# Kernel tuning notes

Hardware: AMD Instinct MI355X
Metric: run time of the kernel (lower is better)

Reference implementation:

```python
import jax, jax.numpy as jnp
import numpy as np

V, D, H, L, B, S = 8192, 128, 8, 2, 1, 128
HD = D // H
HID = int(8 * D / 3)
EPS = 1e-6


def setup_inputs() -> dict:
    key = jax.random.key(0)
    ks = jax.random.split(key, 12)
    sc = 0.02
    return {
        "idx": jax.random.randint(ks[0], (B, S), 0, V),
        "w_raw": jax.random.normal(ks[1], (D, V), jnp.float32) * sc,
        "norm1_w": jnp.ones((L, D), jnp.float32),
        "norm2_w": jnp.ones((L, D), jnp.float32),
        "wq": jax.random.normal(ks[2], (L, D, D), jnp.float32) * sc,
        "wk": jax.random.normal(ks[3], (L, D, D), jnp.float32) * sc,
        "wv": jax.random.normal(ks[4], (L, D, D), jnp.float32) * sc,
        "wo": jax.random.normal(ks[5], (L, D, D), jnp.float32) * sc,
        "w1": jax.random.normal(ks[6], (L, D, HID), jnp.float32) * sc,
        "w3": jax.random.normal(ks[7], (L, D, HID), jnp.float32) * sc,
        "w2": jax.random.normal(ks[8], (L, HID, D), jnp.float32) * sc,
        "final_norm_w": jnp.ones((D,), jnp.float32),
    }


def rmsnorm(x, w):
    return x * jax.lax.rsqrt(jnp.mean(x * x, axis=-1, keepdims=True) + EPS) * w


def rope_cos_sin(seqlen, hd):
    inv = 1.0 / (10000.0 ** (jnp.arange(0, hd, 2, dtype=jnp.float32) / hd))
    t = jnp.arange(seqlen, dtype=jnp.float32)
    f = jnp.outer(t, inv)  # (S, hd/2)
    return jnp.cos(f), jnp.sin(f)


def apply_rope(x, cos, sin):
    # x: (B,S,H,HD); interleaved complex pairs as in Llama
    x0, x1 = x[..., 0::2], x[..., 1::2]
    c = cos[None, :, None, :]
    s = sin[None, :, None, :]
    r0 = x0 * c - x1 * s
    r1 = x0 * s + x1 * c
    return jnp.stack([r0, r1], axis=-1).reshape(x.shape)


def forward(idx, w_raw, norm1_w, norm2_w, wq, wk, wv, wo, w1, w2, w3, final_norm_w):
    Wemb = jax.nn.sigmoid(w_raw)                 # (D,V)
    x = Wemb.T[idx]                              # Yoneda one-hot @ W.T == gather -> (B,S,D)
    cos, sin = rope_cos_sin(S, HD)
    causal = jnp.tril(jnp.ones((S, S), bool))[None, None]  # (1,1,S,S)
    scale = 1.0 / jnp.sqrt(jnp.float32(HD))
    for i in range(L):
        # Multi-Universe attention (heads == universes), RoPE, causal SDPA
        h = rmsnorm(x, norm1_w[i])
        q = (h @ wq[i]).reshape(B, S, H, HD)
        k = (h @ wk[i]).reshape(B, S, H, HD)
        v = (h @ wv[i]).reshape(B, S, H, HD)
        q = apply_rope(q, cos, sin)
        k = apply_rope(k, cos, sin)
        scores = jnp.einsum("bihd,bjhd->bhij", q, k) * scale
        scores = jnp.where(causal, scores, jnp.float32(-1e9))
        attn = jax.nn.softmax(scores, axis=-1)
        o = jnp.einsum("bhij,bjhd->bihd", attn, v).reshape(B, S, D) @ wo[i]
        x = x + o
        # SwiGLU FFN
        h2 = rmsnorm(x, norm2_w[i])
        x = x + (jax.nn.silu(h2 @ w1[i]) * (h2 @ w3[i])) @ w2[i]
    x_norm = rmsnorm(x, final_norm_w)
    # Godel-Heyting reachability head
    x_n = x_norm / jnp.linalg.norm(x_norm, axis=-1, keepdims=True)      # (B,S,D)
    v_n = (Wemb / jnp.linalg.norm(Wemb, axis=0, keepdims=True)).T        # (V,D)
    a = x_n[:, :, None, :]                                               # (B,S,1,D)
    b = v_n[None, None, :, :]                                            # (1,1,V,D)
    # strict Godel implication: a => b = 1 if a <= b else b
    imp = jnp.where(a <= b, jnp.float32(1.0), b)                         # (B,S,V,D)
    logits = jnp.clip(imp.mean(axis=-1), 1e-6, 1.0 - 1e-6)               # (B,S,V)
    return logits


def reference(idx, w_raw, norm1_w, norm2_w, wq, wk, wv, wo, w1, w2, w3, final_norm_w):
    return forward(idx, w_raw, norm1_w, norm2_w, wq, wk, wv, wo, w1, w2, w3, final_norm_w)
```

## Files before the change

kernel.cpp:

```cpp
#include <hip/hip_runtime.h>
#include <math.h>

#define V 8192
#define D 128
#define NH 8
#define HD 16
#define SEQ 128
#define HID 341
#define EPS 1e-6f

__device__ __forceinline__ float sigm(float x) { return 1.0f / (1.0f + expf(-x)); }

__device__ __forceinline__ float block_sum256(float v, float* scratch) {
    #pragma unroll
    for (int m = 32; m > 0; m >>= 1) v += __shfl_xor(v, m);
    if ((threadIdx.x & 63) == 0) scratch[threadIdx.x >> 6] = v;
    __syncthreads();
    float s = (scratch[0] + scratch[1]) + (scratch[2] + scratch[3]);
    __syncthreads();
    return s;
}

__device__ __forceinline__ void qkv_rope(const float* hr, const float* wq,
                                         const float* wk, const float* wv, int s,
                                         float* qrow, float* krow,
                                         float (*vpart)[D], float* qo, float* ko,
                                         float* vo) {
    int t = threadIdx.x;
    int col = t & 127, half = t >> 7;
    {
        const float* w = (t < 128) ? wq : wk;
        float a0 = 0, a1 = 0;
        #pragma unroll 8
        for (int d = 0; d < D; d += 2) {
            a0 += hr[d] * w[d * D + col];
            a1 += hr[d + 1] * w[(d + 1) * D + col];
        }
        if (t < 128) qrow[col] = a0 + a1;
        else krow[col] = a0 + a1;
    }
    {
        int dlo = half * 64;
        float a0 = 0, a1 = 0;
        #pragma unroll 8
        for (int d = dlo; d < dlo + 64; d += 2) {
            a0 += hr[d] * wv[d * D + col];
            a1 += hr[d + 1] * wv[(d + 1) * D + col];
        }
        vpart[half][col] = a0 + a1;
    }
    __syncthreads();
    if (t < 128) {
        vo[s * D + t] = vpart[0][t] + vpart[1][t];
        int c = t & (HD - 1);
        int m = c >> 1;
        float fr = (float)s * expf(-(float)m * 1.15129254649702283e+00f);
        float cs = cosf(fr), sn = sinf(fr);
        int base = t & ~1;
        float qe = qrow[base], qod = qrow[base + 1];
        float ke = krow[base], kod = krow[base + 1];
        qo[s * D + t] = (c & 1) ? (qe * sn + qod * cs) : (qe * cs - qod * sn);
        ko[s * D + t] = (c & 1) ? (ke * sn + kod * cs) : (ke * cs - kod * sn);
    }
}

__global__ __launch_bounds__(256) void k_embed_qkv(
    const int* __restrict__ idx, const float* __restrict__ w_raw,
    const float* __restrict__ wq, const float* __restrict__ wk,
    const float* __restrict__ wv, const float* __restrict__ n1w,
    float* __restrict__ x, float* __restrict__ q, float* __restrict__ k,
    float* __restrict__ v) {
    __shared__ float hr[D], qrow[D], krow[D], vpart[2][D], scr[4];
    int s = blockIdx.x, t = threadIdx.x;
    float xv = 0.f;
    if (t < 128) {
        xv = sigm(w_raw[t * V + idx[s]]);
        x[s * D + t] = xv;
    }
    float ss = block_sum256(xv * xv, scr);
    float r = 1.0f / sqrtf(ss * (1.0f / D) + EPS);
    if (t < 128) hr[t] = xv * r * n1w[t];
    __syncthreads();
    qkv_rope(hr, wq, wk, wv, s, qrow, krow, vpart, q, k, v);
}

template <int MODE>
__global__ __launch_bounds__(256) void k_layer(
    const float* __restrict__ q, const float* __restrict__ kg,
    const float* __restrict__ vg, float* __restrict__ x,
    const float* __restrict__ wo, const float* __restrict__ n2w,
    const float* __restrict__ w1, const float* __restrict__ w3,
    const float* __restrict__ w2, const float* __restrict__ wq,
    const float* __restrict__ wk, const float* __restrict__ wv,
    const float* __restrict__ n1w, float* __restrict__ qo, float* __restrict__ ko,
    float* __restrict__ vo, const float* __restrict__ fw, float* __restrict__ xng) {
    __shared__ float ps[NH][SEQ + 1];
    __shared__ float qs[D], orow[D], h2[D];
    __shared__ float part[2][D];
    __shared__ float qrow[D], krow[D];
    __shared__ float afA[HID], afB[HID], af[HID];
    __shared__ float rl[NH];
    __shared__ float scr[4];
    int s = blockIdx.x, t = threadIdx.x;
    int col = t & 127, half = t >> 7;

    float xr = 0.f;
    if (t < 128) {
        qs[t] = q[s * D + t];
        xr = x[s * D + t];
    }
    __syncthreads();

    {
        int j = col;
        #pragma unroll
        for (int u = 0; u < 4; ++u) {
            int h = half + 2 * u;
            const float4* kp = (const float4*)&kg[j * D + h * HD];
            float4 ka = kp[0], kb = kp[1], kc = kp[2], kd = kp[3];
            const float* qh = &qs[h * HD];
            float acc = ka.x * qh[0] + ka.y * qh[1] + ka.z * qh[2] + ka.w * qh[3] +
                        kb.x * qh[4] + kb.y * qh[5] + kb.z * qh[6] + kb.w * qh[7] +
                        kc.x * qh[8] + kc.y * qh[9] + kc.z * qh[10] + kc.w * qh[11] +
                        kd.x * qh[12] + kd.y * qh[13] + kd.z * qh[14] + kd.w * qh[15];
            ps[h][j] = acc * 0.25f;
        }
    }
    __syncthreads();

    {
        int h = t >> 5, lane = t & 31;
        float pm = -1e30f;
        for (int j = lane; j <= s; j += 32) pm = fmaxf(pm, ps[h][j]);
        #pragma unroll
        for (int m = 16; m > 0; m >>= 1) pm = fmaxf(pm, __shfl_xor(pm, m, 32));
        float psum = 0.f;
        for (int j = lane; j <= s; j += 32) {
            float e = expf(ps[h][j] - pm);
            ps[h][j] = e;
            psum += e;
        }
        #pragma unroll
        for (int m = 16; m > 0; m >>= 1) psum += __shfl_xor(psum, m, 32);
        if (lane == 0) rl[h] = 1.0f / psum;
    }
    __syncthreads();

    {
        int h = col >> 4;
        int jlo = half * 64;
        int jhi = (s < jlo + 63) ? s : (jlo + 63);
        float a0 = 0, a1 = 0, a2 = 0, a3 = 0;
        int j = jlo;
        #pragma unroll 4
        for (; j + 3 <= jhi; j += 4) {
            a0 += ps[h][j] * vg[j * D + col];
            a1 += ps[h][j + 1] * vg[(j + 1) * D + col];
            a2 += ps[h][j + 2] * vg[(j + 2) * D + col];
            a3 += ps[h][j + 3] * vg[(j + 3) * D + col];
        }
        for (; j <= jhi; ++j) a0 += ps[h][j] * vg[j * D + col];
        part[half][col] = (a0 + a1) + (a2 + a3);
    }
    __syncthreads();
    if (t < 128) orow[t] = (part[0][t] + part[1][t]) * rl[t >> 4];
    __syncthreads();

    {
        int dlo = half * 64;
        float a0 = 0, a1 = 0;
        #pragma unroll 8
        for (int d = dlo; d < dlo + 64; d += 2) {
            a0 += orow[d] * wo[d * D + col];
            a1 += orow[d + 1] * wo[(d + 1) * D + col];
        }
        part[half][col] = a0 + a1;
    }
    __syncthreads();
    float xn = 0.f;
    if (t < 128) xn = xr + part[0][t] + part[1][t];
    float ss2 = block_sum256((t < 128) ? xn * xn : 0.f, scr);
    float r2 = 1.0f / sqrtf(ss2 * (1.0f / D) + EPS);
    if (t < 128) h2[t] = xn * r2 * n2w[t];
    __syncthreads();

    for (int task = t; task < 2 * HID; task += 256) {
        int mat = task >= HID;
        int c2 = mat ? (task - HID) : task;
        const float* w = mat ? w3 : w1;
        float a0 = 0, a1 = 0;
        #pragma unroll 8
        for (int d = 0; d < D; d += 2) {
            a0 += h2[d] * w[d * HID + c2];
            a1 += h2[d + 1] * w[(d + 1) * HID + c2];
        }
        if (mat) afB[c2] = a0 + a1;
        else afA[c2] = a0 + a1;
    }
    __syncthreads();
    for (int c2 = t; c2 < HID; c2 += 256) {
        float a1v = afA[c2];
        af[c2] = (a1v / (1.0f + expf(-a1v))) * afB[c2];
    }
    __syncthreads();

    {
        int lo = half * 171;
        int hi = half ? HID : 171;
        float a0 = 0, a1 = 0;
        int tt = lo;
        #pragma unroll 8
        for (; tt + 1 < hi; tt += 2) {
            a0 += af[tt] * w2[tt * D + col];
            a1 += af[tt + 1] * w2[(tt + 1) * D + col];
        }
        for (; tt < hi; ++tt) a0 += af[tt] * w2[tt * D + col];
        part[half][col] = a0 + a1;
    }
    __syncthreads();
    float x2 = 0.f;
    if (t < 128) {
        x2 = xn + part[0][t] + part[1][t];
        if (MODE == 0) x[s * D + t] = x2;
    }

    if constexpr (MODE == 0) {
        float ss = block_sum256((t < 128) ? x2 * x2 : 0.f, scr);
        float r = 1.0f / sqrtf(ss * (1.0f / D) + EPS);
        if (t < 128) h2[t] = x2 * r * n1w[t];
        __syncthreads();
        qkv_rope(h2, wq, wk, wv, s, qrow, krow, part, qo, ko, vo);
    } else {
        float ss = block_sum256((t < 128) ? x2 * x2 : 0.f, scr);
        float r = 1.0f / sqrtf(ss * (1.0f / D) + EPS);
        float y = (t < 128) ? x2 * r * fw[t] : 0.f;
        float nn = block_sum256(y * y, scr);
        if (t < 128) xng[t * SEQ + s] = y / sqrtf(nn);
    }
}

__global__ __launch_bounds__(256) void k_logits(const float* __restrict__ xng,
                                                const float* __restrict__ w_raw,
                                                float* __restrict__ out) {
    __shared__ float xs[D * 64];
    __shared__ float vs[D * 32];
    __shared__ float nred[256];
    __shared__ float invn_s[32];
    int t = threadIdx.x;
    int sbase = (blockIdx.x & 1) * 64;
    int vbase = (blockIdx.x >> 1) * 32;
    for (int i = t; i < D * 64; i += 256) {
        int d = i >> 6, s2 = i & 63;
        xs[i] = xng[d * SEQ + sbase + s2];
    }
    for (int i = t; i < D * 32; i += 256) {
        int d = i >> 5, jj = i & 31;
        vs[i] = sigm(w_raw[d * V + vbase + jj]);
    }
    __syncthreads();
    {
        int colc = t & 31, dp = t >> 5;
        float p = 0.f;
        for (int u = 0; u < 16; ++u) {
            float vv = vs[(dp * 16 + u) * 32 + colc];
            p += vv * vv;
        }
        nred[t] = p;
    }
    __syncthreads();
    if (t < 32) {
        float sum = 0.f;
        for (int u = 0; u < 8; ++u) sum += nred[u * 32 + t];
        invn_s[t] = 1.0f / sqrtf(sum);
    }
    __syncthreads();
    for (int i = t; i < D * 32; i += 256) vs[i] *= invn_s[i & 31];
    __syncthreads();
    int vg = t & 15;
    int sg = t >> 4;
    float acc[4][2] = {};
    for (int d = 0; d < D; ++d) {
        float4 xq = *(const float4*)&xs[d * 64 + sg * 4];
        float2 vq = *(const float2*)&vs[d * 32 + vg * 2];
        acc[0][0] += (xq.x <= vq.x) ? 1.0f : vq.x;
        acc[0][1] += (xq.x <= vq.y) ? 1.0f : vq.y;
        acc[1][0] += (xq.y <= vq.x) ? 1.0f : vq.x;
        acc[1][1] += (xq.y <= vq.y) ? 1.0f : vq.y;
        acc[2][0] += (xq.z <= vq.x) ? 1.0f : vq.x;
        acc[2][1] += (xq.z <= vq.y) ? 1.0f : vq.y;
        acc[3][0] += (xq.w <= vq.x) ? 1.0f : vq.x;
        acc[3][1] += (xq.w <= vq.y) ? 1.0f : vq.y;
    }
    const float inv128 = 1.0f / 128.0f;
    #pragma unroll
    for (int si = 0; si < 4; ++si) {
        int s = sbase + sg * 4 + si;
        float2 ov;
        ov.x = fminf(fmaxf(acc[si][0] * inv128, 1e-6f), 1.0f - 1e-6f);
        ov.y = fminf(fmaxf(acc[si][1] * inv128, 1e-6f), 1.0f - 1e-6f);
        *(float2*)&out[s * V + vbase + vg * 2] = ov;
    }
}

extern "C" void kernel_launch(void* const* d_in, const int* in_sizes, int n_in,
                              void* d_out, int out_size, void* d_ws, size_t ws_size,
                              hipStream_t stream) {
    const int* idx = (const int*)d_in[0];
    const float* w_raw = (const float*)d_in[1];
    const float* n1w = (const float*)d_in[2];
    const float* n2w = (const float*)d_in[3];
    const float* wq = (const float*)d_in[4];
    const float* wk = (const float*)d_in[5];
    const float* wv = (const float*)d_in[6];
    const float* wo = (const float*)d_in[7];
    const float* w1 = (const float*)d_in[8];
    const float* w3 = (const float*)d_in[9];
    const float* w2 = (const float*)d_in[10];
    const float* fnw = (const float*)d_in[11];
    float* out = (float*)d_out;
    float* ws = (float*)d_ws;

    float* x   = ws;
    float* q1  = ws + 16384;
    float* k1  = ws + 32768;
    float* v1  = ws + 49152;
    float* q2  = ws + 65536;
    float* k2  = ws + 81920;
    float* v2  = ws + 98304;
    float* xng = ws + 114688;

    k_embed_qkv<<<dim3(SEQ), dim3(256), 0, stream>>>(idx, w_raw, wq, wk, wv, n1w,
                                                     x, q1, k1, v1);
    k_layer<0><<<dim3(SEQ), dim3(256), 0, stream>>>(
        q1, k1, v1, x, wo, n2w, w1, w3, w2,
        wq + D * D, wk + D * D, wv + D * D, n1w + D, q2, k2, v2,
        (const float*)nullptr, (float*)nullptr);
    k_layer<1><<<dim3(SEQ), dim3(256), 0, stream>>>(
        q2, k2, v2, x, wo + D * D, n2w + D, w1 + D * HID, w3 + D * HID,
        w2 + HID * D, (const float*)nullptr, (const float*)nullptr,
        (const float*)nullptr, (const float*)nullptr, (float*)nullptr,
        (float*)nullptr, (float*)nullptr, fnw, xng);
    k_logits<<<dim3(512), dim3(256), 0, stream>>>(xng, w_raw, out);
}
```

Measured before the change: 159.2 us.

## Coalesce matvecs with float4 loads and shared atomics, precompute vocab norms, prefetch weights

```diff
diff --git a/kernel.cpp b/kernel.cpp
--- a/kernel.cpp
+++ b/kernel.cpp
@@ -9,7 +9,8 @@
 #define HID 341
 #define EPS 1e-6f
 
-__device__ __forceinline__ float sigm(float x) { return 1.0f / (1.0f + expf(-x)); }
+__device__ __forceinline__ float sigm(float x) { return 1.0f / (1.0f + __expf(-x)); }
+__device__ __forceinline__ float silu(float x) { return x / (1.0f + __expf(-x)); }
 
 __device__ __forceinline__ float block_sum256(float v, float* scratch) {
     #pragma unroll
@@ -21,71 +22,98 @@
     return s;
 }
 
-__device__ __forceinline__ void qkv_rope(const float* hr, const float* wq,
-                                         const float* wk, const float* wv, int s,
-                                         float* qrow, float* krow,
-                                         float (*vpart)[D], float* qo, float* ko,
-                                         float* vo) {
+__global__ __launch_bounds__(256, 1) void k_embed_qkv(
+    const int* __restrict__ idx, const float* __restrict__ w_raw,
+    const float* __restrict__ wq, const float* __restrict__ wk,
+    const float* __restrict__ wv, const float* __restrict__ n1w,
+    const float* __restrict__ w1, const float* __restrict__ w3,
+    const float* __restrict__ w2, const float* __restrict__ wo,
+    float* __restrict__ x, float* __restrict__ q, float* __restrict__ k,
+    float* __restrict__ v, float* __restrict__ invn, float* __restrict__ sink) {
     int t = threadIdx.x;
-    int col = t & 127, half = t >> 7;
-    {
-        const float* w = (t < 128) ? wq : wk;
-        float a0 = 0, a1 = 0;
-        #pragma unroll 8
-        for (int d = 0; d < D; d += 2) {
-            a0 += hr[d] * w[d * D + col];
-            a1 += hr[d + 1] * w[(d + 1) * D + col];
-        }
-        if (t < 128) qrow[col] = a0 + a1;
-        else krow[col] = a0 + a1;
-    }
-    {
-        int dlo = half * 64;
-        float a0 = 0, a1 = 0;
-        #pragma unroll 8
-        for (int d = dlo; d < dlo + 64; d += 2) {
-            a0 += hr[d] * wv[d * D + col];
-            a1 += hr[d + 1] * wv[(d + 1) * D + col];
-        }
-        vpart[half][col] = a0 + a1;
-    }
-    __syncthreads();
-    if (t < 128) {
-        vo[s * D + t] = vpart[0][t] + vpart[1][t];
+    if (blockIdx.x >= SEQ) {
+        int vbase = (blockIdx.x - SEQ) * 32;
+        int vloc = t >> 3, dp = t & 7;
+        int vv = vbase + vloc;
+        float acc = 0.f;
+        #pragma unroll
+        for (int u = 0; u < 16; ++u) {
+            float val = sigm(w_raw[(dp * 16 + u) * V + vv]);
+            acc += val * val;
+        }
+        #pragma unroll
+        for (int m = 1; m < 8; m <<= 1) acc += __shfl_xor(acc, m);
+        if (dp == 0) invn[vv] = 1.0f / sqrtf(acc);
+        int g = (blockIdx.x - SEQ) * 256 + t;
+        float wa = 0.f;
+        if (g < 21824) {
+            float4 u1 = ((const float4*)w1)[g]; wa += u1.x + u1.y + u1.z + u1.w;
+            float4 u3 = ((const float4*)w3)[g]; wa += u3.x + u3.y + u3.z + u3.w;
+            float4 u2 = ((const float4*)w2)[g]; wa += u2.x + u2.y + u2.z + u2.w;
+        }
+        if (g < 8192) {
+            float4 a = ((const float4*)wq)[g]; wa += a.x + a.y + a.z + a.w;
+            float4 b = ((const float4*)wk)[g]; wa += b.x + b.y + b.z + b.w;
+            float4 c = ((const float4*)wv)[g]; wa += c.x + c.y + c.z + c.w;
+            float4 d = ((const float4*)wo)[g]; wa += d.x + d.y + d.z + d.w;
+        }
+        if (wa == 1234.5678f) sink[0] = wa;
+        return;
+    }
+    __shared__ float h2[D], qacc[D], kacc[D], vacc[D], scr[4];
+    int s = blockIdx.x;
+    if (t < 128) { qacc[t] = 0.f; kacc[t] = 0.f; vacc[t] = 0.f; }
+    float xv = 0.f;
+    if (t < 128) {
+        xv = sigm(w_raw[t * V + idx[s]]);
+        x[s * D + t] = xv;
+    }
+    float ss = block_sum256(xv * xv, scr);
+    float r = 1.0f / sqrtf(ss * (1.0f / D) + EPS);
+    if (t < 128) h2[t] = xv * r * n1w[t];
+    __syncthreads();
+    {
+        const float4* q4 = (const float4*)wq;
+        const float4* k4 = (const float4*)wk;
+        const float4* v4 = (const float4*)wv;
+        float qa0 = 0, qa1 = 0, qa2 = 0, qa3 = 0;
+        float ka0 = 0, ka1 = 0, ka2 = 0, ka3 = 0;
+        float va0 = 0, va1 = 0, va2 = 0, va3 = 0;
+        #pragma unroll 4
+        for (int j = 0; j < 16; ++j) {
+            int i4 = t + 256 * j;
+            int row = i4 >> 5;
+            float hv = h2[row];
+            float4 a = q4[i4], b = k4[i4], c = v4[i4];
+            qa0 += hv * a.x; qa1 += hv * a.y; qa2 += hv * a.z; qa3 += hv * a.w;
+            ka0 += hv * b.x; ka1 += hv * b.y; ka2 += hv * b.z; ka3 += hv * b.w;
+            va0 += hv * c.x; va1 += hv * c.y; va2 += hv * c.z; va3 += hv * c.w;
+        }
+        int c0 = (t & 31) * 4;
+        atomicAdd(&qacc[c0], qa0); atomicAdd(&qacc[c0 + 1], qa1);
+        atomicAdd(&qacc[c0 + 2], qa2); atomicAdd(&qacc[c0 + 3], qa3);
+        atomicAdd(&kacc[c0], ka0); atomicAdd(&kacc[c0 + 1], ka1);
+        atomicAdd(&kacc[c0 + 2], ka2); atomicAdd(&kacc[c0 + 3], ka3);
+        atomicAdd(&vacc[c0], va0); atomicAdd(&vacc[c0 + 1], va1);
+        atomicAdd(&vacc[c0 + 2], va2); atomicAdd(&vacc[c0 + 3], va3);
+    }
+    __syncthreads();
+    if (t < 128) {
+        v[s * D + t] = vacc[t];
         int c = t & (HD - 1);
         int m = c >> 1;
         float fr = (float)s * expf(-(float)m * 1.15129254649702283e+00f);
         float cs = cosf(fr), sn = sinf(fr);
         int base = t & ~1;
-        float qe = qrow[base], qod = qrow[base + 1];
-        float ke = krow[base], kod = krow[base + 1];
-        qo[s * D + t] = (c & 1) ? (qe * sn + qod * cs) : (qe * cs - qod * sn);
-        ko[s * D + t] = (c & 1) ? (ke * sn + kod * cs) : (ke * cs - kod * sn);
+        float qe = qacc[base], qod = qacc[base + 1];
+        float ke = kacc[base], kod = kacc[base + 1];
+        q[s * D + t] = (c & 1) ? (qe * sn + qod * cs) : (qe * cs - qod * sn);
+        k[s * D + t] = (c & 1) ? (ke * sn + kod * cs) : (ke * cs - kod * sn);
     }
 }
 
-__global__ __launch_bounds__(256) void k_embed_qkv(
-    const int* __restrict__ idx, const float* __restrict__ w_raw,
-    const float* __restrict__ wq, const float* __restrict__ wk,
-    const float* __restrict__ wv, const float* __restrict__ n1w,
-    float* __restrict__ x, float* __restrict__ q, float* __restrict__ k,
-    float* __restrict__ v) {
-    __shared__ float hr[D], qrow[D], krow[D], vpart[2][D], scr[4];
-    int s = blockIdx.x, t = threadIdx.x;
-    float xv = 0.f;
-    if (t < 128) {
-        xv = sigm(w_raw[t * V + idx[s]]);
-        x[s * D + t] = xv;
-    }
-    float ss = block_sum256(xv * xv, scr);
-    float r = 1.0f / sqrtf(ss * (1.0f / D) + EPS);
-    if (t < 128) hr[t] = xv * r * n1w[t];
-    __syncthreads();
-    qkv_rope(hr, wq, wk, wv, s, qrow, krow, vpart, q, k, v);
-}
-
 template <int MODE>
-__global__ __launch_bounds__(256) void k_layer(
+__global__ __launch_bounds__(256, 1) void k_layer(
     const float* __restrict__ q, const float* __restrict__ kg,
     const float* __restrict__ vg, float* __restrict__ x,
     const float* __restrict__ wo, const float* __restrict__ n2w,
@@ -94,16 +122,22 @@
     const float* __restrict__ wk, const float* __restrict__ wv,
     const float* __restrict__ n1w, float* __restrict__ qo, float* __restrict__ ko,
     float* __restrict__ vo, const float* __restrict__ fw, float* __restrict__ xng) {
-    __shared__ float ps[NH][SEQ + 1];
+    __shared__ float ps[NH][SEQ + 2];
     __shared__ float qs[D], orow[D], h2[D];
-    __shared__ float part[2][D];
-    __shared__ float qrow[D], krow[D];
+    __shared__ float oacc[D], pacc[D], qacc[D], kacc[D], vacc[D];
     __shared__ float afA[HID], afB[HID], af[HID];
     __shared__ float rl[NH];
     __shared__ float scr[4];
     int s = blockIdx.x, t = threadIdx.x;
     int col = t & 127, half = t >> 7;
-
+    int cq = t & 31;
+    int c0 = cq * 4;
+
+    if (t < 128) {
+        oacc[t] = 0.f; pacc[t] = 0.f;
+        qacc[t] = 0.f; kacc[t] = 0.f; vacc[t] = 0.f;
+    }
+    for (int i = t; i < HID; i += 256) { afA[i] = 0.f; afB[i] = 0.f; }
     float xr = 0.f;
     if (t < 128) {
         qs[t] = q[s * D + t];
@@ -117,13 +151,13 @@
         for (int u = 0; u < 4; ++u) {
             int h = half + 2 * u;
             const float4* kp = (const float4*)&kg[j * D + h * HD];
-            float4 ka = kp[0], kb = kp[1], kc = kp[2], kd = kp[3];
+            float4 k0 = kp[0], k1 = kp[1], k2 = kp[2], k3 = kp[3];
             const float* qh = &qs[h * HD];
-            float acc = ka.x * qh[0] + ka.y * qh[1] + ka.z * qh[2] + ka.w * qh[3] +
-                        kb.x * qh[4] + kb.y * qh[5] + kb.z * qh[6] + kb.w * qh[7] +
-                        kc.x * qh[8] + kc.y * qh[9] + kc.z * qh[10] + kc.w * qh[11] +
-                        kd.x * qh[12] + kd.y * qh[13] + kd.z * qh[14] + kd.w * qh[15];
-            ps[h][j] = acc * 0.25f;
+            float acc = k0.x * qh[0] + k0.y * qh[1] + k0.z * qh[2] + k0.w * qh[3] +
+                        k1.x * qh[4] + k1.y * qh[5] + k1.z * qh[6] + k1.w * qh[7] +
+                        k2.x * qh[8] + k2.y * qh[9] + k2.z * qh[10] + k2.w * qh[11] +
+                        k3.x * qh[12] + k3.y * qh[13] + k3.z * qh[14] + k3.w * qh[15];
+            ps[h][j] = (j <= s) ? acc * 0.25f : 0.f;
         }
     }
     __syncthreads();
@@ -136,7 +170,7 @@
         for (int m = 16; m > 0; m >>= 1) pm = fmaxf(pm, __shfl_xor(pm, m, 32));
         float psum = 0.f;
         for (int j = lane; j <= s; j += 32) {
-            float e = expf(ps[h][j] - pm);
+            float e = __expf(ps[h][j] - pm);
             ps[h][j] = e;
             psum += e;
         }
@@ -147,93 +181,155 @@
     __syncthreads();
 
     {
-        int h = col >> 4;
-        int jlo = half * 64;
-        int jhi = (s < jlo + 63) ? s : (jlo + 63);
+        const float4* v4 = (const float4*)vg;
+        int h = cq >> 2;
         float a0 = 0, a1 = 0, a2 = 0, a3 = 0;
-        int j = jlo;
-        #pragma unroll 4
-        for (; j + 3 <= jhi; j += 4) {
-            a0 += ps[h][j] * vg[j * D + col];
-            a1 += ps[h][j + 1] * vg[(j + 1) * D + col];
-            a2 += ps[h][j + 2] * vg[(j + 2) * D + col];
-            a3 += ps[h][j + 3] * vg[(j + 3) * D + col];
-        }
-        for (; j <= jhi; ++j) a0 += ps[h][j] * vg[j * D + col];
-        part[half][col] = (a0 + a1) + (a2 + a3);
-    }
-    __syncthreads();
-    if (t < 128) orow[t] = (part[0][t] + part[1][t]) * rl[t >> 4];
-    __syncthreads();
-
-    {
-        int dlo = half * 64;
-        float a0 = 0, a1 = 0;
         #pragma unroll 8
-        for (int d = dlo; d < dlo + 64; d += 2) {
-            a0 += orow[d] * wo[d * D + col];
-            a1 += orow[d + 1] * wo[(d + 1) * D + col];
-        }
-        part[half][col] = a0 + a1;
+        for (int j = 0; j < 16; ++j) {
+            int i4 = t + 256 * j;
+            float p = ps[h][i4 >> 5];
+            float4 vv = v4[i4];
+            a0 += p * vv.x; a1 += p * vv.y; a2 += p * vv.z; a3 += p * vv.w;
+        }
+        atomicAdd(&oacc[c0], a0); atomicAdd(&oacc[c0 + 1], a1);
+        atomicAdd(&oacc[c0 + 2], a2); atomicAdd(&oacc[c0 + 3], a3);
+    }
+    __syncthreads();
+    if (t < 128) {
+        orow[t] = oacc[t] * rl[t >> 4];
+        oacc[t] = 0.f;
+    }
+    __syncthreads();
+
+    {
+        const float4* w4 = (const float4*)wo;
+        float a0 = 0, a1 = 0, a2 = 0, a3 = 0;
+        #pragma unroll 8
+        for (int j = 0; j < 16; ++j) {
+            int i4 = t + 256 * j;
+            float ov = orow[i4 >> 5];
+            float4 ww = w4[i4];
+            a0 += ov * ww.x; a1 += ov * ww.y; a2 += ov * ww.z; a3 += ov * ww.w;
+        }
+        atomicAdd(&pacc[c0], a0); atomicAdd(&pacc[c0 + 1], a1);
+        atomicAdd(&pacc[c0 + 2], a2); atomicAdd(&pacc[c0 + 3], a3);
     }
     __syncthreads();
     float xn = 0.f;
-    if (t < 128) xn = xr + part[0][t] + part[1][t];
+    if (t < 128) xn = xr + pacc[t];
     float ss2 = block_sum256((t < 128) ? xn * xn : 0.f, scr);
     float r2 = 1.0f / sqrtf(ss2 * (1.0f / D) + EPS);
     if (t < 128) h2[t] = xn * r2 * n2w[t];
     __syncthreads();
 
-    for (int task = t; task < 2 * HID; task += 256) {
-        int mat = task >= HID;
-        int c2 = mat ? (task - HID) : task;
-        const float* w = mat ? w3 : w1;
-        float a0 = 0, a1 = 0;
-        #pragma unroll 8
-        for (int d = 0; d < D; d += 2) {
-            a0 += h2[d] * w[d * HID + c2];
-            a1 += h2[d + 1] * w[(d + 1) * HID + c2];
-        }
-        if (mat) afB[c2] = a0 + a1;
-        else afA[c2] = a0 + a1;
-    }
-    __syncthreads();
-    for (int c2 = t; c2 < HID; c2 += 256) {
-        float a1v = afA[c2];
-        af[c2] = (a1v / (1.0f + expf(-a1v))) * afB[c2];
-    }
-    __syncthreads();
-
-    {
-        int lo = half * 171;
-        int hi = half ? HID : 171;
-        float a0 = 0, a1 = 0;
-        int tt = lo;
-        #pragma unroll 8
-        for (; tt + 1 < hi; tt += 2) {
-            a0 += af[tt] * w2[tt * D + col];
-            a1 += af[tt + 1] * w2[(tt + 1) * D + col];
-        }
-        for (; tt < hi; ++tt) a0 += af[tt] * w2[tt * D + col];
-        part[half][col] = a0 + a1;
+    {
+        const float4* w14 = (const float4*)w1;
+        const float4* w34 = (const float4*)w3;
+        #pragma unroll 4
+        for (int j = 0; j < 43; ++j) {
+            int i4 = t + 256 * j;
+            if (i4 < 10912) {
+                float4 a = w14[i4];
+                float4 b = w34[i4];
+                int base = i4 * 4;
+                int d0 = base / HID;
+                int cc = base - d0 * HID;
+                float hv0 = h2[d0];
+                float hv1 = h2[(d0 + 1) & 127];
+                {
+                    atomicAdd(&afA[cc], hv0 * a.x);
+                    atomicAdd(&afB[cc], hv0 * b.x);
+                }
+                {
+                    int c = cc + 1; float hv = hv0;
+                    if (c >= HID) { c -= HID; hv = hv1; }
+                    atomicAdd(&afA[c], hv * a.y);
+                    atomicAdd(&afB[c], hv * b.y);
+                }
+                {
+                    int c = cc + 2; float hv = hv0;
+                    if (c >= HID) { c -= HID; hv = hv1; }
+                    atomicAdd(&afA[c], hv * a.z);
+                    atomicAdd(&afB[c], hv * b.z);
+                }
+                {
+                    int c = cc + 3; float hv = hv0;
+                    if (c >= HID) { c -= HID; hv = hv1; }
+                    atomicAdd(&afA[c], hv * a.w);
+                    atomicAdd(&afB[c], hv * b.w);
+                }
+            }
+        }
+    }
+    __syncthreads();
+    for (int i = t; i < HID; i += 256) af[i] = silu(afA[i]) * afB[i];
+    __syncthreads();
+
+    {
+        const float4* w24 = (const float4*)w2;
+        float a0 = 0, a1 = 0, a2 = 0, a3 = 0;
+        #pragma unroll 4
+        for (int j = 0; j < 43; ++j) {
+            int i4 = t + 256 * j;
+            if (i4 < 10912) {
+                float av = af[i4 >> 5];
+                float4 ww = w24[i4];
+                a0 += av * ww.x; a1 += av * ww.y; a2 += av * ww.z; a3 += av * ww.w;
+            }
+        }
+        atomicAdd(&oacc[c0], a0); atomicAdd(&oacc[c0 + 1], a1);
+        atomicAdd(&oacc[c0 + 2], a2); atomicAdd(&oacc[c0 + 3], a3);
     }
     __syncthreads();
     float x2 = 0.f;
     if (t < 128) {
-        x2 = xn + part[0][t] + part[1][t];
+        x2 = xn + oacc[t];
         if (MODE == 0) x[s * D + t] = x2;
     }
+    float ss3 = block_sum256((t < 128) ? x2 * x2 : 0.f, scr);
+    float r3 = 1.0f / sqrtf(ss3 * (1.0f / D) + EPS);
 
     if constexpr (MODE == 0) {
-        float ss = block_sum256((t < 128) ? x2 * x2 : 0.f, scr);
-        float r = 1.0f / sqrtf(ss * (1.0f / D) + EPS);
-        if (t < 128) h2[t] = x2 * r * n1w[t];
+        if (t < 128) h2[t] = x2 * r3 * n1w[t];
         __syncthreads();
-        qkv_rope(h2, wq, wk, wv, s, qrow, krow, part, qo, ko, vo);
+        {
+            const float4* q4 = (const float4*)wq;
+            const float4* k4 = (const float4*)wk;
+            const float4* v4 = (const float4*)wv;
+            float qa0 = 0, qa1 = 0, qa2 = 0, qa3 = 0;
+            float ka0 = 0, ka1 = 0, ka2 = 0, ka3 = 0;
+            float va0 = 0, va1 = 0, va2 = 0, va3 = 0;
+            #pragma unroll 4
+            for (int j = 0; j < 16; ++j) {
+                int i4 = t + 256 * j;
+                float hv = h2[i4 >> 5];
+                float4 a = q4[i4], b = k4[i4], c = v4[i4];
+                qa0 += hv * a.x; qa1 += hv * a.y; qa2 += hv * a.z; qa3 += hv * a.w;
+                ka0 += hv * b.x; ka1 += hv * b.y; ka2 += hv * b.z; ka3 += hv * b.w;
+                va0 += hv * c.x; va1 += hv * c.y; va2 += hv * c.z; va3 += hv * c.w;
+            }
+            atomicAdd(&qacc[c0], qa0); atomicAdd(&qacc[c0 + 1], qa1);
+            atomicAdd(&qacc[c0 + 2], qa2); atomicAdd(&qacc[c0 + 3], qa3);
+            atomicAdd(&kacc[c0], ka0); atomicAdd(&kacc[c0 + 1], ka1);
+            atomicAdd(&kacc[c0 + 2], ka2); atomicAdd(&kacc[c0 + 3], ka3);
+            atomicAdd(&vacc[c0], va0); atomicAdd(&vacc[c0 + 1], va1);
+            atomicAdd(&vacc[c0 + 2], va2); atomicAdd(&vacc[c0 + 3], va3);
+        }
+        __syncthreads();
+        if (t < 128) {
+            vo[s * D + t] = vacc[t];
+            int c = t & (HD - 1);
+            int mm = c >> 1;
+            float fr = (float)s * expf(-(float)mm * 1.15129254649702283e+00f);
+            float cs = cosf(fr), sn = sinf(fr);
+            int base = t & ~1;
+            float qe = qacc[base], qod = qacc[base + 1];
+            float ke = kacc[base], kod = kacc[base + 1];
+            qo[s * D + t] = (c & 1) ? (qe * sn + qod * cs) : (qe * cs - qod * sn);
+            ko[s * D + t] = (c & 1) ? (ke * sn + kod * cs) : (ke * cs - kod * sn);
+        }
     } else {
-        float ss = block_sum256((t < 128) ? x2 * x2 : 0.f, scr);
-        float r = 1.0f / sqrtf(ss * (1.0f / D) + EPS);
-        float y = (t < 128) ? x2 * r * fw[t] : 0.f;
+        float y = (t < 128) ? x2 * r3 * fw[t] : 0.f;
         float nn = block_sum256(y * y, scr);
         if (t < 128) xng[t * SEQ + s] = y / sqrtf(nn);
     }
@@ -241,11 +337,10 @@
 
 __global__ __launch_bounds__(256) void k_logits(const float* __restrict__ xng,
                                                 const float* __restrict__ w_raw,
+                                                const float* __restrict__ invn,
                                                 float* __restrict__ out) {
     __shared__ float xs[D * 64];
     __shared__ float vs[D * 32];
-    __shared__ float nred[256];
-    __shared__ float invn_s[32];
     int t = threadIdx.x;
     int sbase = (blockIdx.x & 1) * 64;
     int vbase = (blockIdx.x >> 1) * 32;
@@ -255,26 +350,8 @@
     }
     for (int i = t; i < D * 32; i += 256) {
         int d = i >> 5, jj = i & 31;
-        vs[i] = sigm(w_raw[d * V + vbase + jj]);
-    }
-    __syncthreads();
-    {
-        int colc = t & 31, dp = t >> 5;
-        float p = 0.f;
-        for (int u = 0; u < 16; ++u) {
-            float vv = vs[(dp * 16 + u) * 32 + colc];
-            p += vv * vv;
-        }
-        nred[t] = p;
-    }
-    __syncthreads();
-    if (t < 32) {
-        float sum = 0.f;
-        for (int u = 0; u < 8; ++u) sum += nred[u * 32 + t];
-        invn_s[t] = 1.0f / sqrtf(sum);
-    }
-    __syncthreads();
-    for (int i = t; i < D * 32; i += 256) vs[i] *= invn_s[i & 31];
+        vs[i] = sigm(w_raw[d * V + vbase + jj]) * invn[vbase + jj];
+    }
     __syncthreads();
     int vg = t & 15;
     int sg = t >> 4;
@@ -320,17 +397,19 @@
     float* out = (float*)d_out;
     float* ws = (float*)d_ws;
 
-    float* x   = ws;
-    float* q1  = ws + 16384;
-    float* k1  = ws + 32768;
-    float* v1  = ws + 49152;
-    float* q2  = ws + 65536;
-    float* k2  = ws + 81920;
-    float* v2  = ws + 98304;
-    float* xng = ws + 114688;
-
-    k_embed_qkv<<<dim3(SEQ), dim3(256), 0, stream>>>(idx, w_raw, wq, wk, wv, n1w,
-                                                     x, q1, k1, v1);
+    float* x    = ws;
+    float* q1   = ws + 16384;
+    float* k1   = ws + 32768;
+    float* v1   = ws + 49152;
+    float* q2   = ws + 65536;
+    float* k2   = ws + 81920;
+    float* v2   = ws + 98304;
+    float* xng  = ws + 114688;
+    float* sink = ws + 131072;
+    float* invn = ws + 131088;
+
+    k_embed_qkv<<<dim3(SEQ + 256), dim3(256), 0, stream>>>(
+        idx, w_raw, wq, wk, wv, n1w, w1, w3, w2, wo, x, q1, k1, v1, invn, sink);
     k_layer<0><<<dim3(SEQ), dim3(256), 0, stream>>>(
         q1, k1, v1, x, wo, n2w, w1, w3, w2,
         wq + D * D, wk + D * D, wv + D * D, n1w + D, q2, k2, v2,
@@ -340,5 +419,5 @@
         w2 + HID * D, (const float*)nullptr, (const float*)nullptr,
         (const float*)nullptr, (const float*)nullptr, (float*)nullptr,
         (float*)nullptr, (float*)nullptr, fnw, xng);
-    k_logits<<<dim3(512), dim3(256), 0, stream>>>(xng, w_raw, out);
+    k_logits<<<dim3(512), dim3(256), 0, stream>>>(xng, w_raw, invn, out);
 }
```

Measured after the change: 381.0 us. +139.3%, slower.
